# Optimization experiments

Hardware: AMD Instinct MI355X
Metric: run time of the kernel (lower is better)

Reference implementation:

```python
import jax, jax.numpy as jnp
from jax import lax
import numpy as np

# dims
B, P, M = 256, 192, 321
HIDC, HIDR, HIDS = 128, 128, 8
CK, SKIP, HW = 6, 24, 24
SCI_K = 5
PT = (P - CK) // SKIP            # 7
NUM_LEVELS = 3
N_BLOCKS = 2 ** NUM_LEVELS - 1   # 7 Interactor blocks in the tree
PAD = (SCI_K - 1) // 2 + 1       # replication pad = 3 each side (odd kernel)


def setup_inputs() -> dict:
    key = jax.random.key(0)
    ks = jax.random.split(key, 18)
    s = 0.05
    def n(k, shape):
        return jax.random.normal(k, shape, jnp.float32) * s
    return {
        "x": jax.random.normal(ks[0], (B, P, M), jnp.float32),
        # SCINet tree params, stacked: [block, branch(phi,psi,U,P), ...]
        "tree_w1": n(ks[1], (N_BLOCKS, 4, M, M, SCI_K)),
        "tree_b1": n(ks[2], (N_BLOCKS, 4, M)),
        "tree_w2": n(ks[3], (N_BLOCKS, 4, M, M, 3)),
        "tree_b2": n(ks[4], (N_BLOCKS, 4, M)),
        "conv1_w": n(ks[5], (HIDC, 1, CK, M)),
        "conv1_b": n(ks[6], (HIDC,)),
        "gru1_wih": n(ks[7], (3 * HIDR, HIDC)),
        "gru1_whh": n(ks[8], (3 * HIDR, HIDR)),
        "gru1_bih": n(ks[9], (3 * HIDR,)),
        "gru1_bhh": n(ks[10], (3 * HIDR,)),
        "grus_wih": n(ks[11], (3 * HIDS, HIDC)),
        "grus_whh": n(ks[12], (3 * HIDS, HIDS)),
        "grus_bih": n(ks[13], (3 * HIDS,)),
        "grus_bhh": n(ks[14], (3 * HIDS,)),
        "lin1_w": n(ks[15], (M, HIDR + SKIP * HIDS)),
        "lin1_b": n(ks[16], (M,)),
        "hw_w": n(ks[17], (1, HW)),
        "hw_b": jnp.zeros((1,), jnp.float32),
    }


def _conv1d(z, w, b):
    # z: (B, Cin, T), w: (Cout, Cin, K) -> (B, Cout, T-K+1)
    y = lax.conv_general_dilated(z, w, (1,), 'VALID',
                                 dimension_numbers=('NCH', 'OIH', 'NCH'))
    return y + b[None, :, None]


def _gru_last(xs, wih, whh, bih, bhh, hidden):
    # xs: (T, N, I); returns final hidden (N, H). torch GRU gate order r,z,n.
    def step(h, xt):
        gi = xt @ wih.T + bih
        gh = h @ whh.T + bhh
        ir, iz, inn = jnp.split(gi, 3, -1)
        hr, hz, hn = jnp.split(gh, 3, -1)
        r = jax.nn.sigmoid(ir + hr)
        zt = jax.nn.sigmoid(iz + hz)
        nt = jnp.tanh(inn + r * hn)
        return (1.0 - zt) * nt + zt * h, None
    h0 = jnp.zeros((xs.shape[1], hidden), xs.dtype)
    hN, _ = lax.scan(step, h0, xs)
    return hN


def reference(x, tree_w1, tree_b1, tree_w2, tree_b2, conv1_w, conv1_b,
              gru1_wih, gru1_whh, gru1_bih, gru1_bhh,
              grus_wih, grus_whh, grus_bih, grus_bhh,
              lin1_w, lin1_b, hw_w, hw_b):
    def branch(z, i, j):
        # ReplicationPad -> Conv1d k=5 -> LeakyReLU(0.01) -> Conv1d k=3 -> Tanh
        zp = jnp.pad(z, ((0, 0), (0, 0), (PAD, PAD)), mode='edge')
        y = _conv1d(zp, tree_w1[i, j], tree_b1[i, j])
        y = jnp.where(y > 0, y, 0.01 * y)
        y = _conv1d(y, tree_w2[i, j], tree_b2[i, j])
        return jnp.tanh(y)

    counter = [0]
    def tree(z, level):
        # z: (B, T, M). Interactor (INN=True) then recurse / interleave.
        i = counter[0]; counter[0] += 1
        e = z[:, ::2, :].transpose(0, 2, 1)   # (B, M, T/2)
        o = z[:, 1::2, :].transpose(0, 2, 1)
        d = o * jnp.exp(branch(e, i, 0))      # phi
        c = e * jnp.exp(branch(o, i, 1))      # psi
        eu = (c + branch(d, i, 2)).transpose(0, 2, 1)  # U
        ou = (d - branch(c, i, 3)).transpose(0, 2, 1)  # P
        if level > 0:
            eu = tree(eu, level - 1)
            ou = tree(ou, level - 1)
        # zip_up_the_pants: even/odd lengths equal (T divisible by 2^levels)
        b_, l_, m_ = eu.shape
        return jnp.stack([eu, ou], axis=2).reshape(b_, 2 * l_, m_)

    res1 = tree(x, NUM_LEVELS - 1)
    xr = x + res1                              # (B, P, M)

    # Conv2d(1->hidC, kernel (Ck, m)) over (P, m), full-width kernel
    c = lax.conv_general_dilated(xr[:, None, :, :], conv1_w, (1, 1), 'VALID',
                                 dimension_numbers=('NCHW', 'OIHW', 'NCHW'))
    c = jax.nn.relu(c + conv1_b[None, :, None, None])[:, :, :, 0]  # (B,HIDC,L)

    # GRU1 over time
    r = _gru_last(c.transpose(2, 0, 1), gru1_wih, gru1_whh, gru1_bih, gru1_bhh, HIDR)

    # skip GRU
    s = c[:, :, -PT * SKIP:].reshape(B, HIDC, PT, SKIP)
    s = s.transpose(2, 0, 3, 1).reshape(PT, B * SKIP, HIDC)
    s = _gru_last(s, grus_wih, grus_whh, grus_bih, grus_bhh, HIDS)
    s = s.reshape(B, SKIP * HIDS)

    r = jnp.concatenate([r, s], axis=1)
    res = r @ lin1_w.T + lin1_b                # (B, M)

    # highway: AR component over last hw steps per series
    z = xr[:, -HW:, :].transpose(0, 2, 1).reshape(-1, HW)
    z = (z @ hw_w.T + hw_b).reshape(-1, M)
    return res + z
```

## Files before the change

kernel.cpp:

```cpp
#include <hip/hip_runtime.h>
#include <cstddef>
#include <cstdint>

#define Bn 256
#define Pn 192
#define Mn 321
#define Mp 336
#define HIDCn 128
#define HIDRn 128
#define HIDSn 8
#define CKn 6
#define SKIPn 24
#define HWn 24
#define Ln 187
#define PTn 7

typedef _Float16 f16;
typedef f16 f16x2 __attribute__((ext_vector_type(2)));
typedef f16 f16x8 __attribute__((ext_vector_type(8)));
typedef float f32x4 __attribute__((ext_vector_type(4)));
typedef float f32x16 __attribute__((ext_vector_type(16)));

__device__ __forceinline__ float rcpf(float x) {
#if defined(__has_builtin) && __has_builtin(__builtin_amdgcn_rcpf)
  return __builtin_amdgcn_rcpf(x);
#else
  return 1.f / x;
#endif
}
__device__ __forceinline__ float sigmf(float x) { return rcpf(1.f + __expf(-x)); }
__device__ __forceinline__ float tanh_f(float x) {
  float t = __expf(2.f * x);
  return 1.f - 2.f * rcpf(t + 1.f);
}

__device__ __forceinline__ void gll16(const void* g, void* l) {
#if defined(__has_builtin) && __has_builtin(__builtin_amdgcn_global_load_lds)
  __builtin_amdgcn_global_load_lds((const __attribute__((address_space(1))) void*)g,
                                   (__attribute__((address_space(3))) void*)l, 16, 0, 0);
#else
  *(uint4*)l = *(const uint4*)g;
#endif
}

__device__ __forceinline__ int lanepos(int co, int cc) {
  int ctg = co >> 5, row = co & 31;
  int h = (cc >> 3) & 1, d = (cc >> 1) & 3;
  return ((ctg * 256 + h * 128 + row * 4 + d) << 1) | (cc & 1);
}

__global__ __launch_bounds__(256) void repack_w(const float* __restrict__ w, f16* __restrict__ out,
                                                int K, int c0, int c1, int c2) {
  int s = blockIdx.z;
  int n = s >> 2, jj = s & 3;
  int blk = c0 + c1 * n + c2 * (n >> 1);
  int kcib = blockIdx.y;
  int k = kcib / 21, cib = kcib - 21 * k;
  int idx = blockIdx.x * 256 + threadIdx.x;
  int co = idx >> 4, cc = idx & 15;
  int ci = cib * 16 + cc;
  f16 val = (f16)0.f;
  if (co < Mn && ci < Mn)
    val = (f16)w[(((size_t)(blk * 4 + jj) * Mn + co) * Mn + ci) * K + k];
  out[(((size_t)s * K + k) * 21 + cib) * 6144 + lanepos(co, cc)] = val;
}

__global__ __launch_bounds__(256) void repack_c2w(const float* __restrict__ w, f16* __restrict__ out) {
  int idx = blockIdx.x * 256 + threadIdx.x;
  int cc = idx & 15;
  int co = (idx >> 4) & 127;
  int kcib = idx >> 11;
  int k = kcib / 21, cib = kcib - 21 * k;
  int m = cib * 16 + cc;
  f16 v = (f16)0.f;
  if (m < Mn) v = (f16)w[((size_t)co * CKn + k) * Mn + m];
  out[((size_t)(k * 21 + cib)) * 2048 + lanepos(co, cc)] = v;
}

__global__ __launch_bounds__(256) void repack_giw(const float* __restrict__ w, f16* __restrict__ out) {
  int idx = blockIdx.x * 256 + threadIdx.x;
  int cc = idx & 15;
  int co = (idx >> 4) % 384;
  int k = idx / (16 * 384);
  out[(size_t)k * 6144 + lanepos(co, cc)] = (f16)w[(size_t)co * 128 + k * 16 + cc];
}

__global__ __launch_bounds__(256) void deint_k(const float* __restrict__ x32,
                                               const f16* __restrict__ parent, int Thp,
                                               f16* __restrict__ o, int Th) {
  int b = blockIdx.x, t = blockIdx.y, z = blockIdx.z;
  int c = z >> 1, eo = z & 1;
  int srow = 2 * t + eo;
  size_t ooff = (((size_t)z * Bn + b) * Th + t) * Mp;
  if (x32) {
    const float* xp = x32 + ((size_t)b * Pn + srow) * Mn;
    for (int m = threadIdx.x; m < Mp; m += 256)
      o[ooff + m] = (m < Mn) ? (f16)xp[m] : (f16)0.f;
  } else {
    const uint32_t* ip = (const uint32_t*)(parent + (((size_t)c * Bn + b) * Thp + srow) * Mp);
    uint32_t* op = (uint32_t*)(o + ooff);
    for (int i = threadIdx.x; i < Mp / 2; i += 256) op[i] = ip[i];
  }
}

template <int K, int MK>
__global__ __launch_bounds__(512, 2) void conv_mfma(
    const f16* __restrict__ inz, long in_zs, int Tin,
    const f16* __restrict__ Wb, int wc0, int wc1, int wc2, int wjoff,
    const float* __restrict__ biasb,
    const f16* __restrict__ srcz, long src_zs,
    f16* __restrict__ outz, long out_zs, int Tout) {
  constexpr int PADL = (K == 5) ? 3 : 0;
  constexpr int TWIN = 32 + K - 1;
  constexpr int SLAB = K * 21 * 6144;
  constexpr int NS = 21 * K;
  __shared__ __align__(16) f16 sXs[2][4][40][24];
  __shared__ __align__(16) f16 sWs[2][6144];
  int z = blockIdx.z;
  int nnode = z >> 1, j = z & 1;
  int blk = wc0 + wc1 * nnode + wc2 * (nnode >> 1);
  int slot = nnode * 4 + wjoff + j;
  const uint4* inq = (const uint4*)(inz + (size_t)z * in_zs);
  const uint32_t* wsl = (const uint32_t*)(Wb + (size_t)slot * SLAB);
  const float* bias = biasb + (size_t)(blk * 4 + wjoff + j) * Mn;
  int b0 = blockIdx.x * 4;
  int t0 = blockIdx.y * 32;
  int tid = threadIdx.x;
  int lane = tid & 63;
  int wv = tid >> 6;
  int wm = wv & 3, wc = wv >> 2;

  f32x16 acc[6];
#pragma unroll
  for (int i = 0; i < 6; ++i)
#pragma unroll
    for (int q = 0; q < 16; ++q) acc[i][q] = 0.f;

  auto stageX = [&](int cib, int xb) {
    uint32_t* dXu = (uint32_t*)&sXs[xb][0][0][0];
    constexpr int NX4 = 4 * TWIN * 2;
    for (int idx = tid; idx < NX4; idx += 512) {
      int u2 = idx & 1;
      int rr = idx >> 1;
      int tt = rr % TWIN;
      int bl = rr / TWIN;
      int ts = t0 + tt - PADL;
      ts = max(0, min(ts, Tin - 1));
      uint4 v = inq[((((size_t)(b0 + bl)) * Tin + ts) * Mp + cib * 16) / 8 + u2];
      *(uint4*)&dXu[(bl * 40 + tt) * 12 + u2 * 4] = v;
    }
  };
  auto stageW = [&](int s, int wb) {
    int cib = s / K, k = s - cib * K;
    const uint32_t* wp = wsl + ((size_t)(k * 21 + cib)) * 3072;
    uint32_t* dst = (uint32_t*)&sWs[wb][0];
    for (int i = tid; i < 768; i += 512) gll16(wp + i * 4, dst + i * 4);
  };

  stageX(0, 0);
  stageW(0, 0);
  __syncthreads();
  int wb = 0, xb = 0;
#pragma unroll 1
  for (int s = 0; s < NS; ++s) {
    int cib = s / K, k = s - cib * K;
    if (s + 1 < NS) stageW(s + 1, wb ^ 1);
    if (k == K - 1 && cib + 1 < 21) stageX(cib + 1, xb ^ 1);
    f16x8 ah = *(const f16x8*)&sXs[xb][wm][(lane & 31) + k][(lane >> 5) * 8];
    const f16* sw = &sWs[wb][0];
#pragma unroll
    for (int ct = 0; ct < 6; ++ct) {
      f16x8 bw = *(const f16x8*)&sw[((wc * 6 + ct) * 256 + (lane >> 5) * 128 + (lane & 31) * 4) * 2];
      acc[ct] = __builtin_amdgcn_mfma_f32_32x32x16_f16(ah, bw, acc[ct], 0, 0, 0);
    }
    __syncthreads();
    wb ^= 1;
    if (k == K - 1) xb ^= 1;
  }
  f16* o = outz + (size_t)z * out_zs;
  const f16* s = srcz ? srcz + (size_t)(z ^ 1) * src_zs : nullptr;
#pragma unroll
  for (int ct = 0; ct < 6; ++ct) {
    int co = wc * 192 + ct * 32 + (lane & 31);
    if (co >= Mp) continue;
    float bb = (co < Mn) ? bias[co] : 0.f;
#pragma unroll
    for (int r = 0; r < 16; ++r) {
      int row = (r & 3) + 8 * (r >> 2) + 4 * (lane >> 5);
      int t = t0 + row;
      if (t >= Tout) continue;
      size_t oo = (((size_t)(b0 + wm)) * Tout + t) * Mp + co;
      float res;
      if (co >= Mn) {
        res = 0.f;
      } else {
        float v = acc[ct][r] + bb;
        if constexpr (MK == 0) {
          res = v > 0.f ? v : 0.01f * v;
        } else {
          float sv = (float)s[oo];
          float th = tanh_f(v);
          if constexpr (MK == 1) res = sv * __expf(th);
          else res = (j == 0) ? sv + th : sv - th;
        }
      }
      o[oo] = (f16)res;
    }
  }
}

__global__ __launch_bounds__(256) void combine_k(const float* __restrict__ x, const f16* __restrict__ lv,
                                                 float* __restrict__ XR, f16* __restrict__ XRh) {
  int b = blockIdx.x, p = blockIdx.y;
  int c = ((p & 1) << 2) | (p & 2) | ((p >> 2) & 1);
  int row = p >> 3;
  size_t li = (((size_t)c * Bn + b) * 24 + row) * Mp;
  size_t xi = ((size_t)b * Pn + p) * Mn;
  size_t hi = ((size_t)b * Pn + p) * Mp;
  for (int m = threadIdx.x; m < Mp; m += 256) {
    if (m < Mn) {
      float v = x[xi + m] + (float)lv[li + m];
      XR[xi + m] = v;
      XRh[hi + m] = (f16)v;
    } else {
      XRh[hi + m] = (f16)0.f;
    }
  }
}

__global__ __launch_bounds__(256, 4) void conv2d_mfma(
    const f16* __restrict__ xh, const f16* __restrict__ Wh,
    const float* __restrict__ bias, f16* __restrict__ out) {
  __shared__ __align__(16) f16 sXs[2][9][32][24];
  __shared__ __align__(16) f16 sWs[2][2048];
  int b0 = blockIdx.x * 32;
  int l0 = blockIdx.y * 4;
  int tid = threadIdx.x;
  int lane = tid & 63;
  int wv = tid >> 6;

  f32x16 acc[4];
#pragma unroll
  for (int i = 0; i < 4; ++i)
#pragma unroll
    for (int q = 0; q < 16; ++q) acc[i][q] = 0.f;

  const uint4* xq = (const uint4*)xh;

  auto stageX = [&](int cib, int xb) {
    uint32_t* dXu = (uint32_t*)&sXs[xb][0][0][0];
    for (int idx = tid; idx < 576; idx += 256) {
      int u = idx & 1;
      int rr = idx >> 1;
      int bb = rr & 31, tt = rr >> 5;
      int p = min(l0 + tt, Pn - 1);
      uint4 v = xq[((((size_t)(b0 + bb)) * Pn + p) * Mp + cib * 16) / 8 + u];
      *(uint4*)&dXu[(tt * 32 + bb) * 12 + u * 4] = v;
    }
  };
  auto stageW = [&](int s, int wb) {
    int cib = s / CKn, k = s - cib * CKn;
    const uint32_t* wp = (const uint32_t*)(Wh + ((size_t)(k * 21 + cib)) * 2048);
    uint32_t* dst = (uint32_t*)&sWs[wb][0];
    gll16(wp + tid * 4, dst + tid * 4);
  };

  stageX(0, 0);
  stageW(0, 0);
  __syncthreads();
  int wb = 0, xb = 0;
#pragma unroll 1
  for (int s = 0; s < 126; ++s) {
    int cib = s / CKn, k = s - cib * CKn;
    if (s + 1 < 126) stageW(s + 1, wb ^ 1);
    if (k == CKn - 1 && cib + 1 < 21) stageX(cib + 1, xb ^ 1);
    f16x8 ah = *(const f16x8*)&sXs[xb][wv + k][lane & 31][(lane >> 5) * 8];
    const f16* sw = &sWs[wb][0];
#pragma unroll
    for (int ct = 0; ct < 4; ++ct) {
      f16x8 bw = *(const f16x8*)&sw[(ct * 256 + (lane >> 5) * 128 + (lane & 31) * 4) * 2];
      acc[ct] = __builtin_amdgcn_mfma_f32_32x32x16_f16(ah, bw, acc[ct], 0, 0, 0);
    }
    __syncthreads();
    wb ^= 1;
    if (k == CKn - 1) xb ^= 1;
  }
  int l = l0 + wv;
  if (l < Ln) {
#pragma unroll
    for (int ct = 0; ct < 4; ++ct) {
      int co = ct * 32 + (lane & 31);
      float bb = bias[co];
#pragma unroll
      for (int r = 0; r < 16; ++r) {
        int brow = (r & 3) + 8 * (r >> 2) + 4 * (lane >> 5);
        float y = acc[ct][r] + bb;
        out[((size_t)l * Bn + (b0 + brow)) * HIDCn + co] = (f16)(y > 0.f ? y : 0.f);
      }
    }
  }
}

__global__ __launch_bounds__(512, 2) void gemm_gi(const f16* __restrict__ A, const f16* __restrict__ Wb,
                                                  const float* __restrict__ bias, float* __restrict__ out) {
  __shared__ __align__(16) f16 sA[128][136];
  __shared__ __align__(16) f16 sW[2][6144];
  int r0 = blockIdx.x * 128;
  int tid = threadIdx.x;
  int lane = tid & 63;
  int wv = tid >> 6;
  int wm = wv & 3, wc = wv >> 2;

  const uint4* aq = (const uint4*)(A + (size_t)r0 * 128);
  for (int i = tid; i < 2048; i += 512) {
    int row = i >> 4, u = i & 15;
    *(uint4*)&sA[row][u * 8] = aq[i];
  }
  {
    const uint32_t* wp = (const uint32_t*)Wb;
    uint32_t* dst = (uint32_t*)&sW[0][0];
    for (int i = tid; i < 768; i += 512) gll16(wp + i * 4, dst + i * 4);
  }
  __syncthreads();

  f32x16 acc[6];
#pragma unroll
  for (int i = 0; i < 6; ++i)
#pragma unroll
    for (int q = 0; q < 16; ++q) acc[i][q] = 0.f;

  int wb = 0;
#pragma unroll 1
  for (int k = 0; k < 8; ++k) {
    if (k + 1 < 8) {
      const uint32_t* wp = (const uint32_t*)(Wb + (size_t)(k + 1) * 6144);
      uint32_t* dst = (uint32_t*)&sW[wb ^ 1][0];
      for (int i = tid; i < 768; i += 512) gll16(wp + i * 4, dst + i * 4);
    }
    f16x8 ah = *(const f16x8*)&sA[wm * 32 + (lane & 31)][k * 16 + (lane >> 5) * 8];
    const f16* sw = &sW[wb][0];
#pragma unroll
    for (int ct = 0; ct < 6; ++ct) {
      f16x8 bw = *(const f16x8*)&sw[((wc * 6 + ct) * 256 + (lane >> 5) * 128 + (lane & 31) * 4) * 2];
      acc[ct] = __builtin_amdgcn_mfma_f32_32x32x16_f16(ah, bw, acc[ct], 0, 0, 0);
    }
    __syncthreads();
    wb ^= 1;
  }
#pragma unroll
  for (int ct = 0; ct < 6; ++ct) {
    int c = wc * 192 + ct * 32 + (lane & 31);
    float bb = bias[c];
#pragma unroll
    for (int r = 0; r < 16; ++r) {
      int row = r0 + wm * 32 + (r & 3) + 8 * (r >> 2) + 4 * (lane >> 5);
      out[(size_t)row * 384 + c] = acc[ct][r] + bb;
    }
  }
}

__global__ __launch_bounds__(512) void gru1_k(const float* __restrict__ gi, const float* __restrict__ whh,
                                              const float* __restrict__ bhh, float* __restrict__ hout) {
  __shared__ __align__(16) uint32_t hp[2][64];
  int n = blockIdx.x;
  int tid = threadIdx.x;
  int w = tid >> 6, l = tid & 63;
  int colg = l & 15, kg = l >> 4;
  int col = w * 16 + colg;

  f16x8 wfr[3][4];
#pragma unroll
  for (int g = 0; g < 3; ++g) {
    const float* wr = whh + (size_t)(g * 128 + col) * 128;
#pragma unroll
    for (int q = 0; q < 4; ++q) {
      const float4* s4 = (const float4*)(wr + q * 32 + kg * 8);
      float4 lo = s4[0], hi = s4[1];
      f16x8 f;
      f[0] = (f16)lo.x; f[1] = (f16)lo.y; f[2] = (f16)lo.z; f[3] = (f16)lo.w;
      f[4] = (f16)hi.x; f[5] = (f16)hi.y; f[6] = (f16)hi.z; f[7] = (f16)hi.w;
      wfr[g][q] = f;
    }
  }
  float bh_r = bhh[col], bh_z = bhh[128 + col], bh_n = bhh[256 + col];
  if (tid < 128) ((uint32_t*)hp)[tid] = 0u;
  float hprev = 0.f;
  float gA0, gA1, gA2, gB0, gB1, gB2;
  {
    const float* gp = gi + (size_t)n * 384;
    gA0 = gp[col]; gA1 = gp[128 + col]; gA2 = gp[256 + col];
    const float* gq = gi + ((size_t)Bn + n) * 384;
    gB0 = gq[col]; gB1 = gq[128 + col]; gB2 = gq[256 + col];
  }
  __syncthreads();

  auto gstep = [&](int T, float& G0, float& G1, float& G2, int RB) {
    float u0 = G0, u1 = G1, u2 = G2;
    if (T + 2 < Ln) {
      const float* gp = gi + ((size_t)(T + 2) * Bn + n) * 384;
      G0 = gp[col]; G1 = gp[128 + col]; G2 = gp[256 + col];
    }
    f32x4 ac0{}, ac1{}, ac2{};
#pragma unroll
    for (int q = 0; q < 4; ++q) {
      f16x8 af = __builtin_bit_cast(f16x8, *(const uint4*)&hp[RB][q * 16 + kg * 4]);
      ac0 = __builtin_amdgcn_mfma_f32_16x16x32_f16(af, wfr[0][q], ac0, 0, 0, 0);
      ac1 = __builtin_amdgcn_mfma_f32_16x16x32_f16(af, wfr[1][q], ac1, 0, 0, 0);
      ac2 = __builtin_amdgcn_mfma_f32_16x16x32_f16(af, wfr[2][q], ac2, 0, 0, 0);
    }
    float rg = sigmf(u0 + bh_r + ac0[0]);
    float zg = sigmf(u1 + bh_z + ac1[0]);
    float ng = tanh_f(u2 + bh_n + rg * ac2[0]);
    float hnew = (1.f - zg) * ng + zg * hprev;
    hprev = hnew;
    float other = __shfl_xor(hnew, 1, 64);
    if (l < 16 && !(l & 1)) {
      f16 a = (f16)hnew, b2 = (f16)other;
      hp[RB ^ 1][w * 8 + (l >> 1)] = (uint32_t)__builtin_bit_cast(unsigned short, a) |
                                     ((uint32_t)__builtin_bit_cast(unsigned short, b2) << 16);
    }
    asm volatile("s_waitcnt lgkmcnt(0)" ::: "memory");
    __builtin_amdgcn_s_barrier();
    asm volatile("" ::: "memory");
  };

#pragma unroll 1
  for (int t = 0; t + 1 < Ln; t += 2) {
    gstep(t, gA0, gA1, gA2, 0);
    gstep(t + 1, gB0, gB1, gB2, 1);
  }
  gstep(Ln - 1, gA0, gA1, gA2, 0);
  if (l < 16) hout[(size_t)n * 128 + col] = hprev;
}

__global__ __launch_bounds__(256) void gis_k(const f16* __restrict__ cc, const float* __restrict__ wih,
                                             const float* __restrict__ bih, float* __restrict__ gi) {
  __shared__ float sx[24 * 128];
  int t = blockIdx.x, b = blockIdx.y;
  int tid = threadIdx.x;
  for (int idx = tid; idx < 24 * 128; idx += 256) {
    int sk = idx >> 7, i = idx & 127;
    int l = 19 + t * 24 + sk;
    sx[idx] = (float)cc[((size_t)l * Bn + b) * HIDCn + i];
  }
  __syncthreads();
  for (int idx = tid; idx < 576; idx += 256) {
    int sk = idx / 24, g = idx - sk * 24;
    float a = bih[g];
    for (int i = 0; i < 128; ++i) a = fmaf(sx[sk * 128 + i], wih[g * 128 + i], a);
    gi[((size_t)t * (Bn * SKIPn) + b * 24 + sk) * 24 + g] = a;
  }
}

__global__ __launch_bounds__(256) void grus_k(const float* __restrict__ gi, const float* __restrict__ whh,
                                              const float* __restrict__ bhh, float* __restrict__ hout) {
  __shared__ float sw[24 * 8];
  __shared__ float sb[24];
  int tid = threadIdx.x;
  int n = blockIdx.x * 256 + tid;
  if (tid < 192) sw[tid] = whh[tid];
  if (tid < 24) sb[tid] = bhh[tid];
  __syncthreads();
  float h[8];
#pragma unroll
  for (int jj = 0; jj < 8; ++jj) h[jj] = 0.f;
  for (int t = 0; t < PTn; ++t) {
    const float* gir = gi + ((size_t)t * (Bn * SKIPn) + n) * 24;
    float gh[24];
#pragma unroll
    for (int g = 0; g < 24; ++g) {
      float a = sb[g];
#pragma unroll
      for (int jj = 0; jj < 8; ++jj) a = fmaf(sw[g * 8 + jj], h[jj], a);
      gh[g] = a;
    }
#pragma unroll
    for (int jj = 0; jj < 8; ++jj) {
      float rg = sigmf(gir[jj] + gh[jj]);
      float zg = sigmf(gir[8 + jj] + gh[8 + jj]);
      float ng = tanh_f(gir[16 + jj] + rg * gh[16 + jj]);
      h[jj] = (1.f - zg) * ng + zg * h[jj];
    }
  }
#pragma unroll
  for (int jj = 0; jj < 8; ++jj) hout[(size_t)n * 8 + jj] = h[jj];
}

__global__ __launch_bounds__(384) void final_k(const float* __restrict__ h1, const float* __restrict__ hsb,
                                               const float* __restrict__ lw, const float* __restrict__ lb,
                                               const float* __restrict__ xr, const float* __restrict__ hww,
                                               const float* __restrict__ hwb, float* __restrict__ out) {
  __shared__ float sr[320];
  __shared__ float shw[24];
  int b = blockIdx.x;
  int tid = threadIdx.x;
  if (tid < 128) sr[tid] = h1[(size_t)b * 128 + tid];
  else if (tid < 320) sr[tid] = hsb[(size_t)b * 192 + (tid - 128)];
  if (tid >= 320 && tid < 344) shw[tid - 320] = hww[tid - 320];
  __syncthreads();
  int m = tid;
  if (m >= Mn) return;
  float a = lb[m];
  const float* wr = lw + (size_t)m * 320;
  for (int c = 0; c < 320; ++c) a = fmaf(sr[c], wr[c], a);
  float z = hwb[0];
  const float* xrr = xr + ((size_t)b * Pn + (Pn - HWn)) * Mn + m;
#pragma unroll
  for (int k = 0; k < HWn; ++k) z = fmaf(xrr[(size_t)k * Mn], shw[k], z);
  out[(size_t)b * Mn + m] = a + z;
}

extern "C" void kernel_launch(void* const* d_in, const int* in_sizes, int n_in,
                              void* d_out, int out_size, void* d_ws, size_t ws_size,
                              hipStream_t stream) {
  const float* x = (const float*)d_in[0];
  const float* tw1 = (const float*)d_in[1];
  const float* tb1 = (const float*)d_in[2];
  const float* tw2 = (const float*)d_in[3];
  const float* tb2 = (const float*)d_in[4];
  const float* c1w = (const float*)d_in[5];
  const float* c1b = (const float*)d_in[6];
  const float* g1wih = (const float*)d_in[7];
  const float* g1whh = (const float*)d_in[8];
  const float* g1bih = (const float*)d_in[9];
  const float* g1bhh = (const float*)d_in[10];
  const float* gswih = (const float*)d_in[11];
  const float* gswhh = (const float*)d_in[12];
  const float* gsbih = (const float*)d_in[13];
  const float* gsbhh = (const float*)d_in[14];
  const float* l1w = (const float*)d_in[15];
  const float* l1b = (const float*)d_in[16];
  const float* hww = (const float*)d_in[17];
  const float* hwb = (const float*)d_in[18];
  float* out = (float*)d_out;

  const size_t Ah = 17891328ull, Bh = 17891328ull, Ch = 17203200ull;
  f16* Aq = (f16*)d_ws;
  f16* Bq = Aq + Ah;
  f16* Cq = Bq + Bh;
  f16* Wl1 = Cq + Ch;
  f16* Wl2 = Wl1 + 10321920ull;
  f16* Wc2 = (f16*)(Wl2 + 6193152ull);
  f16* Wgi = Wc2 + 258048ull;
  float* giA = (float*)(Wl2 + 6193152ull) + 246528ull;
  float* h1 = giA + 18382848ull;
  float* hsb = h1 + (size_t)Bn * HIDRn;
  float* gis = hsb + (size_t)Bn * SKIPn * HIDSn;
  float* XR = (float*)Bq;
  f16* Cch = Aq;
  f16* XRh = Wl1;

  f16* EO[3] = {Aq, Aq, Bq};
  f16* S1[3] = {Bq, Cq, Aq};
  f16* CD[3] = {Cq, Bq, Cq};
  f16* S3[3] = {Aq, Aq, Bq};
  f16* EU[3] = {Bq, Cq, Aq};
  const int WC0[3] = {0, 1, 2}, WC1[3] = {0, 3, 1}, WC2[3] = {0, 0, 1};

  repack_c2w<<<dim3(1008), 256, 0, stream>>>(c1w, Wc2);
  repack_giw<<<dim3(192), 256, 0, stream>>>(g1wih, Wgi);

  for (int L = 0; L < 3; ++L) {
    int NL = 1 << L;
    int Th = 96 >> L;
    int Z = 2 * NL;
    long zsEO = (long)Bn * Th * Mp;
    long zsS1 = (long)Bn * (Th + 2) * Mp;
    repack_w<<<dim3(24, 5 * 21, NL * 4), 256, 0, stream>>>(tw1, Wl1, 5, WC0[L], WC1[L], WC2[L]);
    repack_w<<<dim3(24, 3 * 21, NL * 4), 256, 0, stream>>>(tw2, Wl2, 3, WC0[L], WC1[L], WC2[L]);
    if (L == 0)
      deint_k<<<dim3(Bn, Th, 2), 256, 0, stream>>>(x, nullptr, 0, EO[0], Th);
    else
      deint_k<<<dim3(Bn, Th, Z), 256, 0, stream>>>(nullptr, EU[L - 1], 2 * Th, EO[L], Th);
    int ty1 = (Th + 2 + 31) / 32, ty2 = (Th + 31) / 32;
    conv_mfma<5, 0><<<dim3(64, ty1, Z), 512, 0, stream>>>(
        EO[L], zsEO, Th, Wl1, WC0[L], WC1[L], WC2[L], 0, tb1,
        nullptr, 0, S1[L], zsS1, Th + 2);
    conv_mfma<3, 1><<<dim3(64, ty2, Z), 512, 0, stream>>>(
        S1[L], zsS1, Th + 2, Wl2, WC0[L], WC1[L], WC2[L], 0, tb2,
        EO[L], zsEO, CD[L], zsEO, Th);
    conv_mfma<5, 0><<<dim3(64, ty1, Z), 512, 0, stream>>>(
        CD[L], zsEO, Th, Wl1, WC0[L], WC1[L], WC2[L], 2, tb1,
        nullptr, 0, S3[L], zsS1, Th + 2);
    conv_mfma<3, 2><<<dim3(64, ty2, Z), 512, 0, stream>>>(
        S3[L], zsS1, Th + 2, Wl2, WC0[L], WC1[L], WC2[L], 2, tb2,
        CD[L], zsEO, EU[L], zsEO, Th);
  }

  combine_k<<<dim3(Bn, Pn), 256, 0, stream>>>(x, EU[2], XR, XRh);

  conv2d_mfma<<<dim3(Bn / 32, (Ln + 3) / 4), 256, 0, stream>>>(XRh, Wc2, c1b, Cch);
  gemm_gi<<<dim3((Ln * Bn) / 128), 512, 0, stream>>>(Cch, Wgi, g1bih, giA);
  gru1_k<<<dim3(Bn), 512, 0, stream>>>(giA, g1whh, g1bhh, h1);
  gis_k<<<dim3(PTn, Bn), 256, 0, stream>>>(Cch, gswih, gsbih, gis);
  grus_k<<<dim3((Bn * SKIPn) / 256), 256, 0, stream>>>(gis, gswhh, gsbhh, hsb);
  final_k<<<dim3(Bn), 384, 0, stream>>>(h1, hsb, l1w, l1b, XR, hww, hwb, out);
}
```

Before: 1.718 ms.

## Fuse deinterleave into conv epilogue and merge GRU tail kernels

The last conv of each tree level now writes its output directly in even/odd-deinterleaved layout for the next level, which removes the separate deint_k copy pass for levels 1 and 2. Buffer assignments are rotated so these in-place layouts do not alias. The GRU1, skip-GRU input projection, skip GRU and final linear/highway kernels are merged into one per-batch tail kernel that keeps intermediates in shared memory. This cuts launches and global round trips, but the skip-GRU recurrence now runs on only 24 threads per block after GRU1 finishes.

```diff
diff --git a/kernel.cpp b/kernel.cpp
--- a/kernel.cpp
+++ b/kernel.cpp
@@ -86,21 +86,14 @@
 }
 
 __global__ __launch_bounds__(256) void deint_k(const float* __restrict__ x32,
-                                               const f16* __restrict__ parent, int Thp,
                                                f16* __restrict__ o, int Th) {
   int b = blockIdx.x, t = blockIdx.y, z = blockIdx.z;
-  int c = z >> 1, eo = z & 1;
+  int eo = z & 1;
   int srow = 2 * t + eo;
   size_t ooff = (((size_t)z * Bn + b) * Th + t) * Mp;
-  if (x32) {
-    const float* xp = x32 + ((size_t)b * Pn + srow) * Mn;
-    for (int m = threadIdx.x; m < Mp; m += 256)
-      o[ooff + m] = (m < Mn) ? (f16)xp[m] : (f16)0.f;
-  } else {
-    const uint32_t* ip = (const uint32_t*)(parent + (((size_t)c * Bn + b) * Thp + srow) * Mp);
-    uint32_t* op = (uint32_t*)(o + ooff);
-    for (int i = threadIdx.x; i < Mp / 2; i += 256) op[i] = ip[i];
-  }
+  const float* xp = x32 + ((size_t)b * Pn + srow) * Mn;
+  for (int m = threadIdx.x; m < Mp; m += 256)
+    o[ooff + m] = (m < Mn) ? (f16)xp[m] : (f16)0.f;
 }
 
 template <int K, int MK>
@@ -109,7 +102,7 @@
     const f16* __restrict__ Wb, int wc0, int wc1, int wc2, int wjoff,
     const float* __restrict__ biasb,
     const f16* __restrict__ srcz, long src_zs,
-    f16* __restrict__ outz, long out_zs, int Tout) {
+    f16* __restrict__ outz, long out_zs, int Tout, int dmode) {
   constexpr int PADL = (K == 5) ? 3 : 0;
   constexpr int TWIN = 32 + K - 1;
   constexpr int SLAB = K * 21 * 6144;
@@ -177,7 +170,7 @@
     wb ^= 1;
     if (k == K - 1) xb ^= 1;
   }
-  f16* o = outz + (size_t)z * out_zs;
+  f16* o = outz + (dmode ? (size_t)0 : (size_t)z * out_zs);
   const f16* s = srcz ? srcz + (size_t)(z ^ 1) * src_zs : nullptr;
 #pragma unroll
   for (int ct = 0; ct < 6; ++ct) {
@@ -189,7 +182,7 @@
       int row = (r & 3) + 8 * (r >> 2) + 4 * (lane >> 5);
       int t = t0 + row;
       if (t >= Tout) continue;
-      size_t oo = (((size_t)(b0 + wm)) * Tout + t) * Mp + co;
+      size_t osrc = (((size_t)(b0 + wm)) * Tout + t) * Mp + co;
       float res;
       if (co >= Mn) {
         res = 0.f;
@@ -198,13 +191,18 @@
         if constexpr (MK == 0) {
           res = v > 0.f ? v : 0.01f * v;
         } else {
-          float sv = (float)s[oo];
+          float sv = (float)s[osrc];
           float th = tanh_f(v);
           if constexpr (MK == 1) res = sv * __expf(th);
           else res = (j == 0) ? sv + th : sv - th;
         }
       }
-      o[oo] = (f16)res;
+      size_t odst = osrc;
+      if constexpr (MK == 2) {
+        if (dmode)
+          odst = (((size_t)(2 * z + (t & 1)) * Bn + (b0 + wm)) * (Tout >> 1) + (t >> 1)) * Mp + co;
+      }
+      o[odst] = (f16)res;
     }
   }
 }
@@ -359,9 +357,20 @@
   }
 }
 
-__global__ __launch_bounds__(512) void gru1_k(const float* __restrict__ gi, const float* __restrict__ whh,
-                                              const float* __restrict__ bhh, float* __restrict__ hout) {
+__global__ __launch_bounds__(512) void tail_k(
+    const float* __restrict__ gi, const float* __restrict__ whh, const float* __restrict__ bhh,
+    const f16* __restrict__ cc, const float* __restrict__ swih, const float* __restrict__ sbih,
+    const float* __restrict__ swhh, const float* __restrict__ sbhh,
+    const float* __restrict__ lw, const float* __restrict__ lb,
+    const float* __restrict__ xr, const float* __restrict__ hww, const float* __restrict__ hwb,
+    float* __restrict__ out) {
   __shared__ __align__(16) uint32_t hp[2][64];
+  __shared__ float hfL[128];
+  __shared__ float gisb[PTn][24][24];
+  __shared__ float hsbL[192];
+  __shared__ float ssw[192];
+  __shared__ float ssb[24];
+  __shared__ float shw[24];
   int n = blockIdx.x;
   int tid = threadIdx.x;
   int w = tid >> 6, l = tid & 63;
@@ -384,6 +393,7 @@
   }
   float bh_r = bhh[col], bh_z = bhh[128 + col], bh_n = bhh[256 + col];
   if (tid < 128) ((uint32_t*)hp)[tid] = 0u;
+  if (tid >= 320 && tid < 344) shw[tid - 320] = hww[tid - 320];
   float hprev = 0.f;
   float gA0, gA1, gA2, gB0, gB1, gB2;
   {
@@ -430,84 +440,66 @@
     gstep(t + 1, gB0, gB1, gB2, 1);
   }
   gstep(Ln - 1, gA0, gA1, gA2, 0);
-  if (l < 16) hout[(size_t)n * 128 + col] = hprev;
-}
-
-__global__ __launch_bounds__(256) void gis_k(const f16* __restrict__ cc, const float* __restrict__ wih,
-                                             const float* __restrict__ bih, float* __restrict__ gi) {
-  __shared__ float sx[24 * 128];
-  int t = blockIdx.x, b = blockIdx.y;
-  int tid = threadIdx.x;
-  for (int idx = tid; idx < 24 * 128; idx += 256) {
-    int sk = idx >> 7, i = idx & 127;
-    int l = 19 + t * 24 + sk;
-    sx[idx] = (float)cc[((size_t)l * Bn + b) * HIDCn + i];
-  }
-  __syncthreads();
-  for (int idx = tid; idx < 576; idx += 256) {
-    int sk = idx / 24, g = idx - sk * 24;
-    float a = bih[g];
-    for (int i = 0; i < 128; ++i) a = fmaf(sx[sk * 128 + i], wih[g * 128 + i], a);
-    gi[((size_t)t * (Bn * SKIPn) + b * 24 + sk) * 24 + g] = a;
-  }
-}
-
-__global__ __launch_bounds__(256) void grus_k(const float* __restrict__ gi, const float* __restrict__ whh,
-                                              const float* __restrict__ bhh, float* __restrict__ hout) {
-  __shared__ float sw[24 * 8];
-  __shared__ float sb[24];
-  int tid = threadIdx.x;
-  int n = blockIdx.x * 256 + tid;
-  if (tid < 192) sw[tid] = whh[tid];
-  if (tid < 24) sb[tid] = bhh[tid];
-  __syncthreads();
-  float h[8];
-#pragma unroll
-  for (int jj = 0; jj < 8; ++jj) h[jj] = 0.f;
-  for (int t = 0; t < PTn; ++t) {
-    const float* gir = gi + ((size_t)t * (Bn * SKIPn) + n) * 24;
-    float gh[24];
-#pragma unroll
-    for (int g = 0; g < 24; ++g) {
-      float a = sb[g];
-#pragma unroll
-      for (int jj = 0; jj < 8; ++jj) a = fmaf(sw[g * 8 + jj], h[jj], a);
-      gh[g] = a;
-    }
-#pragma unroll
-    for (int jj = 0; jj < 8; ++jj) {
-      float rg = sigmf(gir[jj] + gh[jj]);
-      float zg = sigmf(gir[8 + jj] + gh[8 + jj]);
-      float ng = tanh_f(gir[16 + jj] + rg * gh[16 + jj]);
-      h[jj] = (1.f - zg) * ng + zg * h[jj];
-    }
-  }
-#pragma unroll
-  for (int jj = 0; jj < 8; ++jj) hout[(size_t)n * 8 + jj] = h[jj];
-}
-
-__global__ __launch_bounds__(384) void final_k(const float* __restrict__ h1, const float* __restrict__ hsb,
-                                               const float* __restrict__ lw, const float* __restrict__ lb,
-                                               const float* __restrict__ xr, const float* __restrict__ hww,
-                                               const float* __restrict__ hwb, float* __restrict__ out) {
-  __shared__ float sr[320];
-  __shared__ float shw[24];
-  int b = blockIdx.x;
-  int tid = threadIdx.x;
-  if (tid < 128) sr[tid] = h1[(size_t)b * 128 + tid];
-  else if (tid < 320) sr[tid] = hsb[(size_t)b * 192 + (tid - 128)];
-  if (tid >= 320 && tid < 344) shw[tid - 320] = hww[tid - 320];
-  __syncthreads();
+  if (l < 16) hfL[col] = hprev;
+  __syncthreads();
+
+  for (int idx = tid; idx < PTn * 576; idx += 512) {
+    int t = idx / 576, r2 = idx - t * 576;
+    int sk = r2 / 24, g = r2 - sk * 24;
+    const f16* cr = cc + ((size_t)(19 + t * 24 + sk) * Bn + n) * HIDCn;
+    const float* wr = swih + (size_t)g * 128;
+    float a = sbih[g];
+#pragma unroll 4
+    for (int i8 = 0; i8 < 16; ++i8) {
+      f16x8 c8 = *(const f16x8*)(cr + i8 * 8);
+#pragma unroll
+      for (int u = 0; u < 8; ++u) a = fmaf((float)c8[u], wr[i8 * 8 + u], a);
+    }
+    gisb[t][sk][g] = a;
+  }
+  if (tid < 192) ssw[tid] = swhh[tid];
+  if (tid < 24) ssb[tid] = sbhh[tid];
+  __syncthreads();
+
+  if (tid < 24) {
+    int sk = tid;
+    float h[8];
+#pragma unroll
+    for (int jj = 0; jj < 8; ++jj) h[jj] = 0.f;
+    for (int t = 0; t < PTn; ++t) {
+      float gh[24];
+#pragma unroll
+      for (int g = 0; g < 24; ++g) {
+        float a = ssb[g];
+#pragma unroll
+        for (int jj = 0; jj < 8; ++jj) a = fmaf(ssw[g * 8 + jj], h[jj], a);
+        gh[g] = a;
+      }
+#pragma unroll
+      for (int jj = 0; jj < 8; ++jj) {
+        float rg = sigmf(gisb[t][sk][jj] + gh[jj]);
+        float zg = sigmf(gisb[t][sk][8 + jj] + gh[8 + jj]);
+        float ng = tanh_f(gisb[t][sk][16 + jj] + rg * gh[16 + jj]);
+        h[jj] = (1.f - zg) * ng + zg * h[jj];
+      }
+    }
+#pragma unroll
+    for (int jj = 0; jj < 8; ++jj) hsbL[sk * 8 + jj] = h[jj];
+  }
+  __syncthreads();
+
   int m = tid;
-  if (m >= Mn) return;
-  float a = lb[m];
-  const float* wr = lw + (size_t)m * 320;
-  for (int c = 0; c < 320; ++c) a = fmaf(sr[c], wr[c], a);
-  float z = hwb[0];
-  const float* xrr = xr + ((size_t)b * Pn + (Pn - HWn)) * Mn + m;
-#pragma unroll
-  for (int k = 0; k < HWn; ++k) z = fmaf(xrr[(size_t)k * Mn], shw[k], z);
-  out[(size_t)b * Mn + m] = a + z;
+  if (m < Mn) {
+    float a = lb[m];
+    const float* wr = lw + (size_t)m * 320;
+    for (int c = 0; c < 128; ++c) a = fmaf(hfL[c], wr[c], a);
+    for (int c = 0; c < 192; ++c) a = fmaf(hsbL[c], wr[128 + c], a);
+    float zv = hwb[0];
+    const float* xrr = xr + ((size_t)n * Pn + (Pn - HWn)) * Mn + m;
+#pragma unroll
+    for (int k = 0; k < HWn; ++k) zv = fmaf(xrr[(size_t)k * Mn], shw[k], zv);
+    out[(size_t)n * Mn + m] = a + zv;
+  }
 }
 
 extern "C" void kernel_launch(void* const* d_in, const int* in_sizes, int n_in,
@@ -543,18 +535,15 @@
   f16* Wc2 = (f16*)(Wl2 + 6193152ull);
   f16* Wgi = Wc2 + 258048ull;
   float* giA = (float*)(Wl2 + 6193152ull) + 246528ull;
-  float* h1 = giA + 18382848ull;
-  float* hsb = h1 + (size_t)Bn * HIDRn;
-  float* gis = hsb + (size_t)Bn * SKIPn * HIDSn;
-  float* XR = (float*)Bq;
-  f16* Cch = Aq;
+  float* XR = (float*)Aq;
+  f16* Cch = Cq;
   f16* XRh = Wl1;
 
-  f16* EO[3] = {Aq, Aq, Bq};
+  f16* EO[3] = {Aq, Bq, Cq};
   f16* S1[3] = {Bq, Cq, Aq};
-  f16* CD[3] = {Cq, Bq, Cq};
-  f16* S3[3] = {Aq, Aq, Bq};
-  f16* EU[3] = {Bq, Cq, Aq};
+  f16* CD[3] = {Cq, Aq, Bq};
+  f16* S3[3] = {Aq, Bq, Aq};
+  f16* EUF = Cq;
   const int WC0[3] = {0, 1, 2}, WC1[3] = {0, 3, 1}, WC2[3] = {0, 0, 1};
 
   repack_c2w<<<dim3(1008), 256, 0, stream>>>(c1w, Wc2);
@@ -569,30 +558,32 @@
     repack_w<<<dim3(24, 5 * 21, NL * 4), 256, 0, stream>>>(tw1, Wl1, 5, WC0[L], WC1[L], WC2[L]);
     repack_w<<<dim3(24, 3 * 21, NL * 4), 256, 0, stream>>>(tw2, Wl2, 3, WC0[L], WC1[L], WC2[L]);
     if (L == 0)
-      deint_k<<<dim3(Bn, Th, 2), 256, 0, stream>>>(x, nullptr, 0, EO[0], Th);
-    else
-      deint_k<<<dim3(Bn, Th, Z), 256, 0, stream>>>(nullptr, EU[L - 1], 2 * Th, EO[L], Th);
+      deint_k<<<dim3(Bn, Th, 2), 256, 0, stream>>>(x, EO[0], Th);
     int ty1 = (Th + 2 + 31) / 32, ty2 = (Th + 31) / 32;
     conv_mfma<5, 0><<<dim3(64, ty1, Z), 512, 0, stream>>>(
         EO[L], zsEO, Th, Wl1, WC0[L], WC1[L], WC2[L], 0, tb1,
-        nullptr, 0, S1[L], zsS1, Th + 2);
+        nullptr, 0, S1[L], zsS1, Th + 2, 0);
     conv_mfma<3, 1><<<dim3(64, ty2, Z), 512, 0, stream>>>(
         S1[L], zsS1, Th + 2, Wl2, WC0[L], WC1[L], WC2[L], 0, tb2,
-        EO[L], zsEO, CD[L], zsEO, Th);
+        EO[L], zsEO, CD[L], zsEO, Th, 0);
     conv_mfma<5, 0><<<dim3(64, ty1, Z), 512, 0, stream>>>(
         CD[L], zsEO, Th, Wl1, WC0[L], WC1[L], WC2[L], 2, tb1,
-        nullptr, 0, S3[L], zsS1, Th + 2);
-    conv_mfma<3, 2><<<dim3(64, ty2, Z), 512, 0, stream>>>(
-        S3[L], zsS1, Th + 2, Wl2, WC0[L], WC1[L], WC2[L], 2, tb2,
-        CD[L], zsEO, EU[L], zsEO, Th);
-  }
-
-  combine_k<<<dim3(Bn, Pn), 256, 0, stream>>>(x, EU[2], XR, XRh);
+        nullptr, 0, S3[L], zsS1, Th + 2, 0);
+    if (L < 2) {
+      conv_mfma<3, 2><<<dim3(64, ty2, Z), 512, 0, stream>>>(
+          S3[L], zsS1, Th + 2, Wl2, WC0[L], WC1[L], WC2[L], 2, tb2,
+          CD[L], zsEO, EO[L + 1], 0, Th, 1);
+    } else {
+      conv_mfma<3, 2><<<dim3(64, ty2, Z), 512, 0, stream>>>(
+          S3[L], zsS1, Th + 2, Wl2, WC0[L], WC1[L], WC2[L], 2, tb2,
+          CD[L], zsEO, EUF, zsEO, Th, 0);
+    }
+  }
+
+  combine_k<<<dim3(Bn, Pn), 256, 0, stream>>>(x, EUF, XR, XRh);
 
   conv2d_mfma<<<dim3(Bn / 32, (Ln + 3) / 4), 256, 0, stream>>>(XRh, Wc2, c1b, Cch);
   gemm_gi<<<dim3((Ln * Bn) / 128), 512, 0, stream>>>(Cch, Wgi, g1bih, giA);
-  gru1_k<<<dim3(Bn), 512, 0, stream>>>(giA, g1whh, g1bhh, h1);
-  gis_k<<<dim3(PTn, Bn), 256, 0, stream>>>(Cch, gswih, gsbih, gis);
-  grus_k<<<dim3((Bn * SKIPn) / 256), 256, 0, stream>>>(gis, gswhh, gsbhh, hsb);
-  final_k<<<dim3(Bn), 384, 0, stream>>>(h1, hsb, l1w, l1b, XR, hww, hwb, out);
-}
+  tail_k<<<dim3(Bn), 512, 0, stream>>>(giA, g1whh, g1bhh, Cch, gswih, gsbih,
+                                       gswhh, gsbhh, l1w, l1b, XR, hww, hwb, out);
+}
```

Result: no change. 1.688 ms (-1.8%).
